# Kernel optimization log

Hardware: AMD Instinct MI355X
Metric: run time of the kernel (lower is better)

Reference implementation:

```python
import jax, jax.numpy as jnp
import numpy as np

B, D, K, H, W = 2, 512, 32, 64, 64


def setup_inputs() -> dict:
    key = jax.random.key(0)
    k1, k2, k3 = jax.random.split(key, 3)
    X = jax.random.normal(k1, (B, D, H, W), dtype=jnp.float32)
    std1 = 1.0 / (K * D) ** 0.5
    codewords = jax.random.uniform(k2, (K, D), minval=-std1, maxval=std1, dtype=jnp.float32)
    scale = jax.random.uniform(k3, (D, K), minval=-1.0, maxval=0.0, dtype=jnp.float32)
    return {"X": X, "codewords": codewords, "scale": scale}


def reference(X, codewords, scale):
    # X: [B, D, H, W] -> x: [B, N, D], N = H*W
    Bv, Dv = X.shape[0], X.shape[1]
    x = X.reshape(Bv, Dv, -1).transpose(0, 2, 1)            # [B, N, D]
    # broadcast residual: x[b,n,d] - codewords[k,d], scaled per (d,k)
    residual = (x[:, :, :, None] - codewords.T) * scale     # [B, N, D, K]
    # soft assignment over K codewords
    Q = jax.nn.softmax(-0.5 * jnp.sum(residual * residual, axis=2), axis=2)  # [B, N, K]
    # weighted aggregation over N, normalized by per-codeword mass
    Z_num = jnp.einsum('bnk,bndk->bdk', Q, residual)        # [B, D, K]
    Z_ = Z_num / Q.sum(axis=1)[:, None, :]                  # [B, D, K]
    # L2-normalize along D
    Z = Z_ / jnp.sqrt(jnp.sum(Z_ * Z_, axis=1, keepdims=True))
    return (Z, Q)
```

## Files before the change

kernel.cpp:

```cpp
#include <hip/hip_runtime.h>
#include <math.h>

#define B_DIM 2
#define D_DIM 512
#define K_DIM 32
#define N_DIM 4096

typedef float v2f __attribute__((ext_vector_type(2)));

__device__ __forceinline__ void pk_bl(v2f& d, v2f a, v2f b) {
    asm("v_pk_fma_f32 %0, %1, %2, %0 op_sel:[0,0,0] op_sel_hi:[1,0,1]"
        : "+v"(d) : "v"(a), "v"(b));
}
__device__ __forceinline__ void pk_bh(v2f& d, v2f a, v2f b) {
    asm("v_pk_fma_f32 %0, %1, %2, %0 op_sel:[0,1,0] op_sel_hi:[1,1,1]"
        : "+v"(d) : "v"(a), "v"(b));
}

__global__ __launch_bounds__(256)
void k_prep(const float* __restrict__ CW, const float* __restrict__ SC,
            float* __restrict__ A, float* __restrict__ B2,
            float* __restrict__ CK, float* __restrict__ zeroes)
{
    __shared__ float ckred[8][33];
    const int tid = threadIdx.x;
    const int idx = blockIdx.x * 256 + tid;
    const int d = idx >> 5, k = idx & 31;
    float s = SC[idx];
    float c = CW[k * D_DIM + d];
    float a = s * s;
    A[idx]  = a;
    B2[idx] = -2.f * a * c;
    if (blockIdx.x == 0) {
        if (tid < 128) zeroes[tid] = 0.f;
        const int kk = tid & 31, g = tid >> 5;
        float acc = 0.f;
        for (int dd = g * 64; dd < g * 64 + 64; ++dd) {
            float sv = SC[dd * K_DIM + kk];
            float cv = CW[kk * D_DIM + dd];
            acc = fmaf(sv * sv * cv, cv, acc);
        }
        ckred[g][kk] = acc;
        __syncthreads();
        if (tid < 32) {
            float t = 0.f;
#pragma unroll
            for (int i = 0; i < 8; ++i) t += ckred[i][tid];
            CK[tid] = t;
        }
    }
}

__global__ __launch_bounds__(256, 2)
void k_dist_q(const float* __restrict__ X, const float* __restrict__ At,
              const float* __restrict__ Bt, const float* __restrict__ CK,
              float* __restrict__ Qout)
{
    __shared__ __align__(16) float xlds[D_DIM * 16];
    __shared__ __align__(16) float part[8 * 16 * 36];

    const int tid = threadIdx.x;
    const int b  = blockIdx.x >> 8;
    const int n0 = (blockIdx.x & 255) << 4;

    const float* xsrc = X + (size_t)b * D_DIM * N_DIM + n0;
#pragma unroll
    for (int j = 0; j < 8; ++j) {
        const int d  = (tid >> 2) + (j << 6);
        const int n4 = (tid & 3) << 2;
        *(float4*)(&xlds[d * 16 + n4]) =
            *(const float4*)(xsrc + (size_t)d * N_DIM + n4);
    }

    const int ks  = tid & 7;
    const int ng  = (tid >> 3) & 3;
    const int dsl = tid >> 5;

    float acc[4][4];
#pragma unroll
    for (int n = 0; n < 4; ++n)
#pragma unroll
        for (int k = 0; k < 4; ++k) acc[n][k] = 0.f;

    const float* arow = At + ((dsl << 6) * K_DIM) + (ks << 2);
    const float* brow = Bt + ((dsl << 6) * K_DIM) + (ks << 2);
    __syncthreads();
    const float* xrow = &xlds[(dsl << 6) * 16 + (ng << 2)];

    for (int i = 0; i < 64; i += 8) {
#pragma unroll
        for (int u = 0; u < 8; ++u) {
            const int d = i + u;
            float4 a4 = *(const float4*)(arow + d * K_DIM);
            float4 b4 = *(const float4*)(brow + d * K_DIM);
            float4 x4 = *(const float4*)(xrow + d * 16);
            float av[4] = {a4.x, a4.y, a4.z, a4.w};
            float bv[4] = {b4.x, b4.y, b4.z, b4.w};
            float xv[4] = {x4.x, x4.y, x4.z, x4.w};
#pragma unroll
            for (int n = 0; n < 4; ++n) {
                const float x  = xv[n];
                const float x2 = x * x;
#pragma unroll
                for (int k = 0; k < 4; ++k)
                    acc[n][k] = fmaf(av[k], x2, fmaf(bv[k], x, acc[n][k]));
            }
        }
    }

    __syncthreads();
#pragma unroll
    for (int nj = 0; nj < 4; ++nj)
        *(float4*)(&part[(dsl * 16 + (ng << 2) + nj) * 36 + (ks << 2)]) =
            make_float4(acc[nj][0], acc[nj][1], acc[nj][2], acc[nj][3]);
    __syncthreads();

#pragma unroll
    for (int h = 0; h < 2; ++h) {
        const int n = (tid >> 5) + (h << 3);
        const int k = tid & 31;
        float dsum = CK[k];
#pragma unroll
        for (int i = 0; i < 8; ++i) dsum += part[(i * 16 + n) * 36 + k];
        float m = dsum;
#pragma unroll
        for (int mk = 16; mk >= 1; mk >>= 1)
            m = fminf(m, __shfl_xor(m, mk));
        float e = __expf(-0.5f * (dsum - m));
        float ssum = e;
#pragma unroll
        for (int mk = 16; mk >= 1; mk >>= 1)
            ssum += __shfl_xor(ssum, mk);
        Qout[((size_t)b * N_DIM + n0 + n) * K_DIM + k] = __fdividef(e, ssum);
    }
}

__global__ __launch_bounds__(256, 2)
void k_tpart(const float* __restrict__ X, const float* __restrict__ Qin,
             float* __restrict__ TP, float* __restrict__ Mpart)
{
    __shared__ __align__(16) float Xs[64 * 68];
    __shared__ __align__(16) float Qs[64 * 36];
    __shared__ __align__(16) float red4[4 * 64 * 36];
    __shared__ float mred[8][33];

    const int tid = threadIdx.x;
    const int bid = blockIdx.x;
    const int ns = bid & 31;
    const int dt = (bid >> 5) & 7;
    const int b  = bid >> 8;
    const int nsub = tid >> 5;
    const int dp = tid & 7;
    const int kp = (tid >> 3) & 3;
    const int k0t = kp << 3;
    const int wv = tid >> 6;

    v2f acc2[8][4];
#pragma unroll
    for (int i = 0; i < 8; ++i)
#pragma unroll
        for (int j = 0; j < 4; ++j) acc2[i][j] = (v2f)(0.f);

    const float* xsrc = X + ((size_t)b * D_DIM + dt * 64) * N_DIM + ns * 128;
    const float* qsrc = Qin + ((size_t)b * N_DIM + ns * 128) * K_DIM;

    for (int ch = 0; ch < 2; ++ch) {
        __syncthreads();
#pragma unroll
        for (int i = 0; i < 4; ++i) {
            int flat4 = tid + (i << 8);
            int row = flat4 >> 4;
            int c4  = (flat4 & 15) << 2;
            float4 v = *(const float4*)(xsrc + (size_t)row * N_DIM + (ch << 6) + c4);
            *(float4*)(&Xs[row * 68 + c4]) = v;
        }
#pragma unroll
        for (int i = 0; i < 2; ++i) {
            int flat4 = tid + (i << 8);
            int nn = flat4 >> 3;
            int k4 = (flat4 & 7) << 2;
            *(float4*)(&Qs[nn * 36 + k4]) =
                *(const float4*)(qsrc + ((ch << 6) + nn) * K_DIM + k4);
        }
        __syncthreads();
#pragma unroll
        for (int s = 0; s < 2; ++s) {
            const int nb = (nsub << 3) + (s << 2);
            float4 xr[8];
#pragma unroll
            for (int i = 0; i < 8; ++i)
                xr[i] = *(const float4*)(&Xs[(dp + (i << 3)) * 68 + nb]);
#pragma unroll
            for (int n = 0; n < 4; ++n) {
                float4 qa = *(const float4*)(&Qs[(nb + n) * 36 + k0t]);
                float4 qb = *(const float4*)(&Qs[(nb + n) * 36 + k0t + 4]);
                v2f q2[4] = {{qa.x, qa.y}, {qa.z, qa.w}, {qb.x, qb.y}, {qb.z, qb.w}};
#pragma unroll
                for (int i = 0; i < 8; ++i) {
                    v2f xlo = {xr[i].x, xr[i].y};
                    v2f xhi = {xr[i].z, xr[i].w};
                    v2f xb2 = (n < 2) ? xlo : xhi;
                    if ((n & 1) == 0) {
#pragma unroll
                        for (int j = 0; j < 4; ++j) pk_bl(acc2[i][j], q2[j], xb2);
                    } else {
#pragma unroll
                        for (int j = 0; j < 4; ++j) pk_bh(acc2[i][j], q2[j], xb2);
                    }
                }
            }
        }
    }
    __syncthreads();
#pragma unroll
    for (int i = 0; i < 8; ++i)
#pragma unroll
        for (int j = 0; j < 4; ++j) {
            acc2[i][j].x += __shfl_xor(acc2[i][j].x, 32);
            acc2[i][j].y += __shfl_xor(acc2[i][j].y, 32);
        }
    if ((tid & 32) == 0) {
#pragma unroll
        for (int i = 0; i < 8; ++i) {
            float* r = &red4[(wv * 64 + dp + (i << 3)) * 36 + k0t];
            *(float4*)(r)     = make_float4(acc2[i][0].x, acc2[i][0].y,
                                            acc2[i][1].x, acc2[i][1].y);
            *(float4*)(r + 4) = make_float4(acc2[i][2].x, acc2[i][2].y,
                                            acc2[i][3].x, acc2[i][3].y);
        }
    }
    __syncthreads();
    float* dst = TP + (((size_t)ns * 2 + b) * D_DIM + dt * 64) * K_DIM;
#pragma unroll
    for (int e = 0; e < 8; ++e) {
        int flat = tid + (e << 8);
        int dl = flat >> 5;
        int k  = flat & 31;
        float s = red4[(0 * 64 + dl) * 36 + k] + red4[(1 * 64 + dl) * 36 + k]
                + red4[(2 * 64 + dl) * 36 + k] + red4[(3 * 64 + dl) * 36 + k];
        dst[dl * K_DIM + k] = s;
    }
    if (dt == 0) {
        const int k = tid & 31, g = tid >> 5;
        float qm = 0.f;
#pragma unroll
        for (int n = 0; n < 16; ++n)
            qm += qsrc[(g * 16 + n) * K_DIM + k];
        mred[g][k] = qm;
        __syncthreads();
        if (tid < K_DIM) {
            float t = 0.f;
#pragma unroll
            for (int i = 0; i < 8; ++i) t += mred[i][tid];
            Mpart[(ns * B_DIM + b) * K_DIM + tid] = t;
        }
    }
}

__global__ __launch_bounds__(256)
void k_zfuse(const float* __restrict__ TP, const float* __restrict__ Mpart,
             const float* __restrict__ CW, const float* __restrict__ SC,
             float* __restrict__ Z, float* __restrict__ nsq, int* __restrict__ cnt)
{
    __shared__ float part[8][33];
    const int tid = threadIdx.x;
    const int b  = blockIdx.x >> 6;
    const int ds = blockIdx.x & 63;
    const int d  = (ds << 3) + (tid >> 5);
    const int k  = tid & 31;
    float sum = 0.f;
#pragma unroll
    for (int ns = 0; ns < 32; ++ns)
        sum += TP[(((size_t)ns * 2 + b) * D_DIM + d) * K_DIM + k];
    float m = 0.f;
#pragma unroll
    for (int ns = 0; ns < 32; ++ns)
        m += Mpart[(ns * B_DIM + b) * K_DIM + k];
    float c = CW[k * D_DIM + d];
    float s = SC[d * K_DIM + k];
    float z = s * (sum / m - c);
    part[tid >> 5][k] = z * z;
    __syncthreads();
    if (tid < K_DIM) {
        float t = 0.f;
#pragma unroll
        for (int i = 0; i < 8; ++i) t += part[i][tid];
        atomicAdd(&nsq[b * K_DIM + tid], t);
    }
    __syncthreads();
    if (tid == 0) {
        __hip_atomic_fetch_add(cnt, 1, __ATOMIC_ACQ_REL, __HIP_MEMORY_SCOPE_AGENT);
        while (__hip_atomic_load(cnt, __ATOMIC_ACQUIRE, __HIP_MEMORY_SCOPE_AGENT) < 128)
            __builtin_amdgcn_s_sleep(1);
    }
    __syncthreads();
    float nv = __hip_atomic_load(&nsq[b * K_DIM + k], __ATOMIC_RELAXED,
                                 __HIP_MEMORY_SCOPE_AGENT);
    Z[((b * D_DIM) + d) * K_DIM + k] = z * rsqrtf(nv);
}

extern "C" void kernel_launch(void* const* d_in, const int* in_sizes, int n_in,
                              void* d_out, int out_size, void* d_ws, size_t ws_size,
                              hipStream_t stream)
{
    const float* X  = (const float*)d_in[0];
    const float* CW = (const float*)d_in[1];
    const float* SC = (const float*)d_in[2];
    float* Z = (float*)d_out;
    float* Q = (float*)d_out + B_DIM * D_DIM * K_DIM;

    float* W    = (float*)d_ws;
    float* nsq  = W;
    int*   cnt  = (int*)(W + 64);
    float* Mpart= W + 128;
    float* TP   = W + 128 + 2048;
    float* At   = TP + 32 * B_DIM * D_DIM * K_DIM;
    float* Bt   = At + D_DIM * K_DIM;
    float* CKt  = Bt + D_DIM * K_DIM;

    k_prep  <<< 64, 256, 0, stream>>>(CW, SC, At, Bt, CKt, W);
    k_dist_q<<<512, 256, 0, stream>>>(X, At, Bt, CKt, Q);
    k_tpart <<<512, 256, 0, stream>>>(X, Q, TP, Mpart);
    k_zfuse <<<128, 256, 0, stream>>>(TP, Mpart, CW, SC, Z, nsq, cnt);
}
```

Before: 102.8 us.

## Split distance kernel into D-sliced partial pass plus separate softmax kernel

The fused distance-plus-softmax kernel is split in two. The first kernel computes partial squared distances over 64-row D slabs for 64-point N tiles, with smaller LDS use and higher occupancy, and writes 8 partial slabs to a workspace buffer. A new softmax kernel sums those slabs, applies the softmax, writes Q and computes the per-codeword mass partials that k_tpart used to compute. This trades extra global traffic (about 8 MB of partials written and read back) and one more launch for better occupancy and less redundant A/B reloads in the distance pass.

```diff
diff --git a/kernel.cpp b/kernel.cpp
--- a/kernel.cpp
+++ b/kernel.cpp
@@ -51,30 +51,36 @@
     }
 }
 
-__global__ __launch_bounds__(256, 2)
-void k_dist_q(const float* __restrict__ X, const float* __restrict__ At,
-              const float* __restrict__ Bt, const float* __restrict__ CK,
-              float* __restrict__ Qout)
-{
-    __shared__ __align__(16) float xlds[D_DIM * 16];
-    __shared__ __align__(16) float part[8 * 16 * 36];
-
-    const int tid = threadIdx.x;
+__global__ __launch_bounds__(256, 4)
+void k_dist(const float* __restrict__ X, const float* __restrict__ At,
+            const float* __restrict__ Bt, float* __restrict__ DB)
+{
+    __shared__ __align__(16) float xs[128 * 68];
+
+    const int tid = threadIdx.x;
+    const int nb = blockIdx.x & 63;
+    const int dc = (blockIdx.x >> 6) & 3;
     const int b  = blockIdx.x >> 8;
-    const int n0 = (blockIdx.x & 255) << 4;
-
-    const float* xsrc = X + (size_t)b * D_DIM * N_DIM + n0;
-#pragma unroll
-    for (int j = 0; j < 8; ++j) {
-        const int d  = (tid >> 2) + (j << 6);
-        const int n4 = (tid & 3) << 2;
-        *(float4*)(&xlds[d * 16 + n4]) =
-            *(const float4*)(xsrc + (size_t)d * N_DIM + n4);
-    }
-
-    const int ks  = tid & 7;
-    const int ng  = (tid >> 3) & 3;
-    const int dsl = tid >> 5;
+
+    const float* xsrc = X + ((size_t)b * D_DIM + dc * 128) * N_DIM + nb * 64;
+#pragma unroll
+    for (int i = 0; i < 8; ++i) {
+        int flat4 = tid + (i << 8);
+        int row  = flat4 >> 4;
+        int col4 = (flat4 & 15) << 2;
+        *(float4*)(&xs[row * 68 + col4]) =
+            *(const float4*)(xsrc + (size_t)row * N_DIM + col4);
+    }
+    __syncthreads();
+
+    const int ks = tid & 7;
+    const int ng = (tid >> 3) & 15;
+    const int dh = tid >> 7;
+    const int d0 = dc * 128 + dh * 64;
+
+    const float* ar = At + d0 * K_DIM + (ks << 2);
+    const float* br = Bt + d0 * K_DIM + (ks << 2);
+    const float* xr = &xs[(dh << 6) * 68 + (ng << 2)];
 
     float acc[4][4];
 #pragma unroll
@@ -82,67 +88,80 @@
 #pragma unroll
         for (int k = 0; k < 4; ++k) acc[n][k] = 0.f;
 
-    const float* arow = At + ((dsl << 6) * K_DIM) + (ks << 2);
-    const float* brow = Bt + ((dsl << 6) * K_DIM) + (ks << 2);
-    __syncthreads();
-    const float* xrow = &xlds[(dsl << 6) * 16 + (ng << 2)];
-
-    for (int i = 0; i < 64; i += 8) {
-#pragma unroll
-        for (int u = 0; u < 8; ++u) {
-            const int d = i + u;
-            float4 a4 = *(const float4*)(arow + d * K_DIM);
-            float4 b4 = *(const float4*)(brow + d * K_DIM);
-            float4 x4 = *(const float4*)(xrow + d * 16);
-            float av[4] = {a4.x, a4.y, a4.z, a4.w};
-            float bv[4] = {b4.x, b4.y, b4.z, b4.w};
-            float xv[4] = {x4.x, x4.y, x4.z, x4.w};
-#pragma unroll
-            for (int n = 0; n < 4; ++n) {
-                const float x  = xv[n];
-                const float x2 = x * x;
-#pragma unroll
-                for (int k = 0; k < 4; ++k)
-                    acc[n][k] = fmaf(av[k], x2, fmaf(bv[k], x, acc[n][k]));
-            }
-        }
-    }
-
-    __syncthreads();
-#pragma unroll
-    for (int nj = 0; nj < 4; ++nj)
-        *(float4*)(&part[(dsl * 16 + (ng << 2) + nj) * 36 + (ks << 2)]) =
-            make_float4(acc[nj][0], acc[nj][1], acc[nj][2], acc[nj][3]);
-    __syncthreads();
-
-#pragma unroll
-    for (int h = 0; h < 2; ++h) {
-        const int n = (tid >> 5) + (h << 3);
-        const int k = tid & 31;
-        float dsum = CK[k];
-#pragma unroll
-        for (int i = 0; i < 8; ++i) dsum += part[(i * 16 + n) * 36 + k];
-        float m = dsum;
+#pragma unroll 8
+    for (int d = 0; d < 64; ++d) {
+        float4 a4 = *(const float4*)(ar + d * K_DIM);
+        float4 b4 = *(const float4*)(br + d * K_DIM);
+        float4 x4 = *(const float4*)(xr + d * 68);
+        float av[4] = {a4.x, a4.y, a4.z, a4.w};
+        float bv[4] = {b4.x, b4.y, b4.z, b4.w};
+        float xv[4] = {x4.x, x4.y, x4.z, x4.w};
+#pragma unroll
+        for (int n = 0; n < 4; ++n) {
+            const float x  = xv[n];
+            const float x2 = x * x;
+#pragma unroll
+            for (int k = 0; k < 4; ++k)
+                acc[n][k] = fmaf(av[k], x2, fmaf(bv[k], x, acc[n][k]));
+        }
+    }
+
+    const int slab = dc * 2 + dh;
+    float* dst = DB + (((size_t)slab * B_DIM + b) * N_DIM + nb * 64 + (ng << 2))
+                    * K_DIM + (ks << 2);
+#pragma unroll
+    for (int nn = 0; nn < 4; ++nn)
+        *(float4*)(dst + nn * K_DIM) =
+            make_float4(acc[nn][0], acc[nn][1], acc[nn][2], acc[nn][3]);
+}
+
+__global__ __launch_bounds__(256)
+void k_softmax(const float* __restrict__ DB, const float* __restrict__ CK,
+               float* __restrict__ Qout, float* __restrict__ Mpart)
+{
+    __shared__ float mred[8][33];
+    const int tid = threadIdx.x;
+    const int b  = blockIdx.x >> 6;
+    const int nb = blockIdx.x & 63;
+    const int k = tid & 31, g = tid >> 5;
+    float qm = 0.f;
+#pragma unroll
+    for (int p = 0; p < 8; ++p) {
+        const int n = nb * 64 + p * 8 + g;
+        float s = CK[k];
+#pragma unroll
+        for (int sl = 0; sl < 8; ++sl)
+            s += DB[(((size_t)sl * B_DIM + b) * N_DIM + n) * K_DIM + k];
+        float m = s;
 #pragma unroll
         for (int mk = 16; mk >= 1; mk >>= 1)
             m = fminf(m, __shfl_xor(m, mk));
-        float e = __expf(-0.5f * (dsum - m));
+        float e = __expf(-0.5f * (s - m));
         float ssum = e;
 #pragma unroll
         for (int mk = 16; mk >= 1; mk >>= 1)
             ssum += __shfl_xor(ssum, mk);
-        Qout[((size_t)b * N_DIM + n0 + n) * K_DIM + k] = __fdividef(e, ssum);
+        float q = __fdividef(e, ssum);
+        Qout[((size_t)b * N_DIM + n) * K_DIM + k] = q;
+        qm += q;
+    }
+    mred[g][k] = qm;
+    __syncthreads();
+    if (tid < K_DIM) {
+        float t = 0.f;
+#pragma unroll
+        for (int i = 0; i < 8; ++i) t += mred[i][tid];
+        Mpart[blockIdx.x * K_DIM + tid] = t;
     }
 }
 
 __global__ __launch_bounds__(256, 2)
 void k_tpart(const float* __restrict__ X, const float* __restrict__ Qin,
-             float* __restrict__ TP, float* __restrict__ Mpart)
+             float* __restrict__ TP)
 {
     __shared__ __align__(16) float Xs[64 * 68];
     __shared__ __align__(16) float Qs[64 * 36];
     __shared__ __align__(16) float red4[4 * 64 * 36];
-    __shared__ float mred[8][33];
 
     const int tid = threadIdx.x;
     const int bid = blockIdx.x;
@@ -240,21 +259,6 @@
                 + red4[(2 * 64 + dl) * 36 + k] + red4[(3 * 64 + dl) * 36 + k];
         dst[dl * K_DIM + k] = s;
     }
-    if (dt == 0) {
-        const int k = tid & 31, g = tid >> 5;
-        float qm = 0.f;
-#pragma unroll
-        for (int n = 0; n < 16; ++n)
-            qm += qsrc[(g * 16 + n) * K_DIM + k];
-        mred[g][k] = qm;
-        __syncthreads();
-        if (tid < K_DIM) {
-            float t = 0.f;
-#pragma unroll
-            for (int i = 0; i < 8; ++i) t += mred[i][tid];
-            Mpart[(ns * B_DIM + b) * K_DIM + tid] = t;
-        }
-    }
 }
 
 __global__ __launch_bounds__(256)
@@ -274,8 +278,8 @@
         sum += TP[(((size_t)ns * 2 + b) * D_DIM + d) * K_DIM + k];
     float m = 0.f;
 #pragma unroll
-    for (int ns = 0; ns < 32; ++ns)
-        m += Mpart[(ns * B_DIM + b) * K_DIM + k];
+    for (int i = 0; i < 64; ++i)
+        m += Mpart[((b << 6) + i) * K_DIM + k];
     float c = CW[k * D_DIM + d];
     float s = SC[d * K_DIM + k];
     float z = s * (sum / m - c);
@@ -313,13 +317,15 @@
     float* nsq  = W;
     int*   cnt  = (int*)(W + 64);
     float* Mpart= W + 128;
-    float* TP   = W + 128 + 2048;
-    float* At   = TP + 32 * B_DIM * D_DIM * K_DIM;
+    float* TP   = Mpart + 4096;
+    float* DB   = TP + 32 * B_DIM * D_DIM * K_DIM;
+    float* At   = DB + 8 * B_DIM * N_DIM * K_DIM;
     float* Bt   = At + D_DIM * K_DIM;
     float* CKt  = Bt + D_DIM * K_DIM;
 
-    k_prep  <<< 64, 256, 0, stream>>>(CW, SC, At, Bt, CKt, W);
-    k_dist_q<<<512, 256, 0, stream>>>(X, At, Bt, CKt, Q);
-    k_tpart <<<512, 256, 0, stream>>>(X, Q, TP, Mpart);
-    k_zfuse <<<128, 256, 0, stream>>>(TP, Mpart, CW, SC, Z, nsq, cnt);
-}
+    k_prep   <<< 64, 256, 0, stream>>>(CW, SC, At, Bt, CKt, W);
+    k_dist   <<<512, 256, 0, stream>>>(X, At, Bt, DB);
+    k_softmax<<<128, 256, 0, stream>>>(DB, CKt, Q, Mpart);
+    k_tpart  <<<512, 256, 0, stream>>>(X, Q, TP);
+    k_zfuse  <<<128, 256, 0, stream>>>(TP, Mpart, CW, SC, Z, nsq, cnt);
+}
```

Measured after the change: 106.4 us. 1.04x slower.

## Fuse distance/softmax, aggregation and normalization into one persistent kernel with grid barriers

Applied to the files above, without the earlier changes.

Merges the three main kernels (distance plus softmax, Q-weighted aggregation, and Z normalization) into a single 256-block persistent kernel separated by atomic-counter grid barriers. The per-codeword mass is now accumulated atomically during the softmax stage instead of being reduced separately. Each block handles 32 tokens in the first phase and two aggregation tiles in the second. This removes two kernel launches and their gaps, at the cost of lower occupancy (one block per CU), spin-wait barriers that assume all 256 blocks are co-resident, and a non-deterministic order for the atomic reductions.

```diff
diff --git a/kernel.cpp b/kernel.cpp
--- a/kernel.cpp
+++ b/kernel.cpp
@@ -17,10 +17,20 @@
         : "+v"(d) : "v"(a), "v"(b));
 }
 
+__device__ __forceinline__ void gridbar(int* cnt, int target) {
+    __syncthreads();
+    if (threadIdx.x == 0) {
+        __hip_atomic_fetch_add(cnt, 1, __ATOMIC_ACQ_REL, __HIP_MEMORY_SCOPE_AGENT);
+        while (__hip_atomic_load(cnt, __ATOMIC_ACQUIRE, __HIP_MEMORY_SCOPE_AGENT) < target)
+            __builtin_amdgcn_s_sleep(2);
+    }
+    __syncthreads();
+}
+
 __global__ __launch_bounds__(256)
 void k_prep(const float* __restrict__ CW, const float* __restrict__ SC,
             float* __restrict__ A, float* __restrict__ B2,
-            float* __restrict__ CK, float* __restrict__ zeroes)
+            float* __restrict__ CK, float* __restrict__ W)
 {
     __shared__ float ckred[8][33];
     const int tid = threadIdx.x;
@@ -32,7 +42,7 @@
     A[idx]  = a;
     B2[idx] = -2.f * a * c;
     if (blockIdx.x == 0) {
-        if (tid < 128) zeroes[tid] = 0.f;
+        if (tid < 136) W[tid] = 0.f;
         const int kk = tid & 31, g = tid >> 5;
         float acc = 0.f;
         for (int dd = g * 64; dd < g * 64 + 64; ++dd) {
@@ -51,49 +61,48 @@
     }
 }
 
-__global__ __launch_bounds__(256, 2)
-void k_dist_q(const float* __restrict__ X, const float* __restrict__ At,
-              const float* __restrict__ Bt, const float* __restrict__ CK,
-              float* __restrict__ Qout)
+__global__ __launch_bounds__(256, 1)
+void k_mega(const float* __restrict__ X, const float* __restrict__ CW,
+            const float* __restrict__ SC, const float* __restrict__ At,
+            const float* __restrict__ Bt, const float* __restrict__ CK,
+            float* __restrict__ Qout, float* __restrict__ Z,
+            float* __restrict__ W, float* __restrict__ TP)
 {
-    __shared__ __align__(16) float xlds[D_DIM * 16];
-    __shared__ __align__(16) float part[8 * 16 * 36];
-
+    __shared__ __align__(16) float sm[18432];
+    float* Mv  = W;
+    float* nsq = W + 64;
+    int*   cnt = (int*)(W + 128);
     const int tid = threadIdx.x;
-    const int b  = blockIdx.x >> 8;
-    const int n0 = (blockIdx.x & 255) << 4;
-
-    const float* xsrc = X + (size_t)b * D_DIM * N_DIM + n0;
-#pragma unroll
-    for (int j = 0; j < 8; ++j) {
-        const int d  = (tid >> 2) + (j << 6);
-        const int n4 = (tid & 3) << 2;
-        *(float4*)(&xlds[d * 16 + n4]) =
-            *(const float4*)(xsrc + (size_t)d * N_DIM + n4);
-    }
-
-    const int ks  = tid & 7;
-    const int ng  = (tid >> 3) & 3;
-    const int dsl = tid >> 5;
-
-    float acc[4][4];
-#pragma unroll
-    for (int n = 0; n < 4; ++n)
-#pragma unroll
-        for (int k = 0; k < 4; ++k) acc[n][k] = 0.f;
-
-    const float* arow = At + ((dsl << 6) * K_DIM) + (ks << 2);
-    const float* brow = Bt + ((dsl << 6) * K_DIM) + (ks << 2);
-    __syncthreads();
-    const float* xrow = &xlds[(dsl << 6) * 16 + (ng << 2)];
-
-    for (int i = 0; i < 64; i += 8) {
-#pragma unroll
-        for (int u = 0; u < 8; ++u) {
-            const int d = i + u;
-            float4 a4 = *(const float4*)(arow + d * K_DIM);
-            float4 b4 = *(const float4*)(brow + d * K_DIM);
-            float4 x4 = *(const float4*)(xrow + d * 16);
+    const int blk = blockIdx.x;
+
+    {
+        const int b  = blk >> 7;
+        const int n0 = (blk & 127) << 5;
+        const float* xsrc = X + (size_t)b * D_DIM * N_DIM + n0;
+#pragma unroll
+        for (int i = 0; i < 16; ++i) {
+            int f4 = tid + (i << 8);
+            int row = f4 >> 3, col4 = (f4 & 7) << 2;
+            *(float4*)(&sm[row * 36 + col4]) =
+                *(const float4*)(xsrc + (size_t)row * N_DIM + col4);
+        }
+        __syncthreads();
+
+        const int ks = tid & 7, ng = (tid >> 3) & 7, dh = tid >> 6;
+        const float* ar = At + (dh << 7) * K_DIM + (ks << 2);
+        const float* br = Bt + (dh << 7) * K_DIM + (ks << 2);
+        const float* xr = &sm[(dh << 7) * 36 + (ng << 2)];
+        float acc[4][4];
+#pragma unroll
+        for (int n = 0; n < 4; ++n)
+#pragma unroll
+            for (int k = 0; k < 4; ++k) acc[n][k] = 0.f;
+
+#pragma unroll 8
+        for (int d = 0; d < 128; ++d) {
+            float4 a4 = *(const float4*)(ar + d * K_DIM);
+            float4 b4 = *(const float4*)(br + d * K_DIM);
+            float4 x4 = *(const float4*)(xr + d * 36);
             float av[4] = {a4.x, a4.y, a4.z, a4.w};
             float bv[4] = {b4.x, b4.y, b4.z, b4.w};
             float xv[4] = {x4.x, x4.y, x4.z, x4.w};
@@ -106,197 +115,187 @@
                     acc[n][k] = fmaf(av[k], x2, fmaf(bv[k], x, acc[n][k]));
             }
         }
-    }
-
-    __syncthreads();
-#pragma unroll
-    for (int nj = 0; nj < 4; ++nj)
-        *(float4*)(&part[(dsl * 16 + (ng << 2) + nj) * 36 + (ks << 2)]) =
-            make_float4(acc[nj][0], acc[nj][1], acc[nj][2], acc[nj][3]);
-    __syncthreads();
-
-#pragma unroll
-    for (int h = 0; h < 2; ++h) {
-        const int n = (tid >> 5) + (h << 3);
+        __syncthreads();
+#pragma unroll
+        for (int nj = 0; nj < 4; ++nj)
+            *(float4*)(&sm[((dh << 5) + (ng << 2) + nj) * 36 + (ks << 2)]) =
+                make_float4(acc[nj][0], acc[nj][1], acc[nj][2], acc[nj][3]);
+        __syncthreads();
+
         const int k = tid & 31;
-        float dsum = CK[k];
-#pragma unroll
-        for (int i = 0; i < 8; ++i) dsum += part[(i * 16 + n) * 36 + k];
-        float m = dsum;
-#pragma unroll
-        for (int mk = 16; mk >= 1; mk >>= 1)
-            m = fminf(m, __shfl_xor(m, mk));
-        float e = __expf(-0.5f * (dsum - m));
-        float ssum = e;
-#pragma unroll
-        for (int mk = 16; mk >= 1; mk >>= 1)
-            ssum += __shfl_xor(ssum, mk);
-        Qout[((size_t)b * N_DIM + n0 + n) * K_DIM + k] = __fdividef(e, ssum);
-    }
-}
-
-__global__ __launch_bounds__(256, 2)
-void k_tpart(const float* __restrict__ X, const float* __restrict__ Qin,
-             float* __restrict__ TP, float* __restrict__ Mpart)
-{
-    __shared__ __align__(16) float Xs[64 * 68];
-    __shared__ __align__(16) float Qs[64 * 36];
-    __shared__ __align__(16) float red4[4 * 64 * 36];
-    __shared__ float mred[8][33];
-
-    const int tid = threadIdx.x;
-    const int bid = blockIdx.x;
-    const int ns = bid & 31;
-    const int dt = (bid >> 5) & 7;
-    const int b  = bid >> 8;
-    const int nsub = tid >> 5;
-    const int dp = tid & 7;
-    const int kp = (tid >> 3) & 3;
-    const int k0t = kp << 3;
-    const int wv = tid >> 6;
-
-    v2f acc2[8][4];
-#pragma unroll
-    for (int i = 0; i < 8; ++i)
-#pragma unroll
-        for (int j = 0; j < 4; ++j) acc2[i][j] = (v2f)(0.f);
-
-    const float* xsrc = X + ((size_t)b * D_DIM + dt * 64) * N_DIM + ns * 128;
-    const float* qsrc = Qin + ((size_t)b * N_DIM + ns * 128) * K_DIM;
-
-    for (int ch = 0; ch < 2; ++ch) {
-        __syncthreads();
-#pragma unroll
-        for (int i = 0; i < 4; ++i) {
-            int flat4 = tid + (i << 8);
-            int row = flat4 >> 4;
-            int c4  = (flat4 & 15) << 2;
-            float4 v = *(const float4*)(xsrc + (size_t)row * N_DIM + (ch << 6) + c4);
-            *(float4*)(&Xs[row * 68 + c4]) = v;
-        }
-#pragma unroll
-        for (int i = 0; i < 2; ++i) {
-            int flat4 = tid + (i << 8);
-            int nn = flat4 >> 3;
-            int k4 = (flat4 & 7) << 2;
-            *(float4*)(&Qs[nn * 36 + k4]) =
-                *(const float4*)(qsrc + ((ch << 6) + nn) * K_DIM + k4);
-        }
-        __syncthreads();
-#pragma unroll
-        for (int s = 0; s < 2; ++s) {
-            const int nb = (nsub << 3) + (s << 2);
-            float4 xr[8];
-#pragma unroll
-            for (int i = 0; i < 8; ++i)
-                xr[i] = *(const float4*)(&Xs[(dp + (i << 3)) * 68 + nb]);
-#pragma unroll
-            for (int n = 0; n < 4; ++n) {
-                float4 qa = *(const float4*)(&Qs[(nb + n) * 36 + k0t]);
-                float4 qb = *(const float4*)(&Qs[(nb + n) * 36 + k0t + 4]);
-                v2f q2[4] = {{qa.x, qa.y}, {qa.z, qa.w}, {qb.x, qb.y}, {qb.z, qb.w}};
-#pragma unroll
-                for (int i = 0; i < 8; ++i) {
-                    v2f xlo = {xr[i].x, xr[i].y};
-                    v2f xhi = {xr[i].z, xr[i].w};
-                    v2f xb2 = (n < 2) ? xlo : xhi;
-                    if ((n & 1) == 0) {
-#pragma unroll
-                        for (int j = 0; j < 4; ++j) pk_bl(acc2[i][j], q2[j], xb2);
-                    } else {
-#pragma unroll
-                        for (int j = 0; j < 4; ++j) pk_bh(acc2[i][j], q2[j], xb2);
-                    }
-                }
-            }
-        }
-    }
-    __syncthreads();
-#pragma unroll
-    for (int i = 0; i < 8; ++i)
-#pragma unroll
-        for (int j = 0; j < 4; ++j) {
-            acc2[i][j].x += __shfl_xor(acc2[i][j].x, 32);
-            acc2[i][j].y += __shfl_xor(acc2[i][j].y, 32);
-        }
-    if ((tid & 32) == 0) {
-#pragma unroll
-        for (int i = 0; i < 8; ++i) {
-            float* r = &red4[(wv * 64 + dp + (i << 3)) * 36 + k0t];
-            *(float4*)(r)     = make_float4(acc2[i][0].x, acc2[i][0].y,
-                                            acc2[i][1].x, acc2[i][1].y);
-            *(float4*)(r + 4) = make_float4(acc2[i][2].x, acc2[i][2].y,
-                                            acc2[i][3].x, acc2[i][3].y);
-        }
-    }
-    __syncthreads();
-    float* dst = TP + (((size_t)ns * 2 + b) * D_DIM + dt * 64) * K_DIM;
-#pragma unroll
-    for (int e = 0; e < 8; ++e) {
-        int flat = tid + (e << 8);
-        int dl = flat >> 5;
-        int k  = flat & 31;
-        float s = red4[(0 * 64 + dl) * 36 + k] + red4[(1 * 64 + dl) * 36 + k]
-                + red4[(2 * 64 + dl) * 36 + k] + red4[(3 * 64 + dl) * 36 + k];
-        dst[dl * K_DIM + k] = s;
-    }
-    if (dt == 0) {
-        const int k = tid & 31, g = tid >> 5;
         float qm = 0.f;
 #pragma unroll
-        for (int n = 0; n < 16; ++n)
-            qm += qsrc[(g * 16 + n) * K_DIM + k];
-        mred[g][k] = qm;
+        for (int h = 0; h < 4; ++h) {
+            const int n = (h << 3) + (tid >> 5);
+            float dsum = CK[k];
+#pragma unroll
+            for (int i = 0; i < 4; ++i) dsum += sm[((i << 5) + n) * 36 + k];
+            float m = dsum;
+#pragma unroll
+            for (int mk = 16; mk >= 1; mk >>= 1)
+                m = fminf(m, __shfl_xor(m, mk));
+            float e = __expf(-0.5f * (dsum - m));
+            float ssum = e;
+#pragma unroll
+            for (int mk = 16; mk >= 1; mk >>= 1)
+                ssum += __shfl_xor(ssum, mk);
+            float q = __fdividef(e, ssum);
+            Qout[((size_t)b * N_DIM + n0 + n) * K_DIM + k] = q;
+            qm += q;
+        }
+        sm[4608 + (tid >> 5) * 33 + k] = qm;
         __syncthreads();
         if (tid < K_DIM) {
             float t = 0.f;
 #pragma unroll
-            for (int i = 0; i < 8; ++i) t += mred[i][tid];
-            Mpart[(ns * B_DIM + b) * K_DIM + tid] = t;
-        }
-    }
-}
-
-__global__ __launch_bounds__(256)
-void k_zfuse(const float* __restrict__ TP, const float* __restrict__ Mpart,
-             const float* __restrict__ CW, const float* __restrict__ SC,
-             float* __restrict__ Z, float* __restrict__ nsq, int* __restrict__ cnt)
-{
-    __shared__ float part[8][33];
-    const int tid = threadIdx.x;
-    const int b  = blockIdx.x >> 6;
-    const int ds = blockIdx.x & 63;
-    const int d  = (ds << 3) + (tid >> 5);
-    const int k  = tid & 31;
-    float sum = 0.f;
-#pragma unroll
-    for (int ns = 0; ns < 32; ++ns)
-        sum += TP[(((size_t)ns * 2 + b) * D_DIM + d) * K_DIM + k];
-    float m = 0.f;
-#pragma unroll
-    for (int ns = 0; ns < 32; ++ns)
-        m += Mpart[(ns * B_DIM + b) * K_DIM + k];
-    float c = CW[k * D_DIM + d];
-    float s = SC[d * K_DIM + k];
-    float z = s * (sum / m - c);
-    part[tid >> 5][k] = z * z;
-    __syncthreads();
-    if (tid < K_DIM) {
+            for (int i = 0; i < 8; ++i) t += sm[4608 + i * 33 + tid];
+            atomicAdd(&Mv[b * K_DIM + tid], t);
+        }
+    }
+    gridbar(&cnt[0], 256);
+
+    {
+        float* Xs   = sm;
+        float* Qs   = sm + 4352;
+        float* red4 = sm + 6656;
+        const int nsub = tid >> 5;
+        const int dp = tid & 7;
+        const int kp = (tid >> 3) & 3;
+        const int k0t = kp << 3;
+        const int wv = tid >> 6;
+
+        for (int a = 0; a < 2; ++a) {
+            const int g  = (blk << 1) | a;
+            const int ns = g & 31;
+            const int dt = (g >> 5) & 7;
+            const int b  = g >> 8;
+
+            v2f acc2[8][4];
+#pragma unroll
+            for (int i = 0; i < 8; ++i)
+#pragma unroll
+                for (int j = 0; j < 4; ++j) acc2[i][j] = (v2f)(0.f);
+
+            const float* xsrc = X + ((size_t)b * D_DIM + dt * 64) * N_DIM + ns * 128;
+            const float* qsrc = Qout + ((size_t)b * N_DIM + ns * 128) * K_DIM;
+
+            for (int ch = 0; ch < 2; ++ch) {
+                __syncthreads();
+#pragma unroll
+                for (int i = 0; i < 4; ++i) {
+                    int flat4 = tid + (i << 8);
+                    int row = flat4 >> 4;
+                    int c4  = (flat4 & 15) << 2;
+                    *(float4*)(&Xs[row * 68 + c4]) =
+                        *(const float4*)(xsrc + (size_t)row * N_DIM + (ch << 6) + c4);
+                }
+#pragma unroll
+                for (int i = 0; i < 2; ++i) {
+                    int flat4 = tid + (i << 8);
+                    int nn = flat4 >> 3;
+                    int k4 = (flat4 & 7) << 2;
+                    *(float4*)(&Qs[nn * 36 + k4]) =
+                        *(const float4*)(qsrc + ((ch << 6) + nn) * K_DIM + k4);
+                }
+                __syncthreads();
+#pragma unroll
+                for (int s = 0; s < 2; ++s) {
+                    const int nb = (nsub << 3) + (s << 2);
+                    float4 xr[8];
+#pragma unroll
+                    for (int i = 0; i < 8; ++i)
+                        xr[i] = *(const float4*)(&Xs[(dp + (i << 3)) * 68 + nb]);
+#pragma unroll
+                    for (int n = 0; n < 4; ++n) {
+                        float4 qa = *(const float4*)(&Qs[(nb + n) * 36 + k0t]);
+                        float4 qb = *(const float4*)(&Qs[(nb + n) * 36 + k0t + 4]);
+                        v2f q2[4] = {{qa.x, qa.y}, {qa.z, qa.w},
+                                     {qb.x, qb.y}, {qb.z, qb.w}};
+#pragma unroll
+                        for (int i = 0; i < 8; ++i) {
+                            v2f xlo = {xr[i].x, xr[i].y};
+                            v2f xhi = {xr[i].z, xr[i].w};
+                            v2f xb2 = (n < 2) ? xlo : xhi;
+                            if ((n & 1) == 0) {
+#pragma unroll
+                                for (int j = 0; j < 4; ++j) pk_bl(acc2[i][j], q2[j], xb2);
+                            } else {
+#pragma unroll
+                                for (int j = 0; j < 4; ++j) pk_bh(acc2[i][j], q2[j], xb2);
+                            }
+                        }
+                    }
+                }
+            }
+            __syncthreads();
+#pragma unroll
+            for (int i = 0; i < 8; ++i)
+#pragma unroll
+                for (int j = 0; j < 4; ++j) {
+                    acc2[i][j].x += __shfl_xor(acc2[i][j].x, 32);
+                    acc2[i][j].y += __shfl_xor(acc2[i][j].y, 32);
+                }
+            if ((tid & 32) == 0) {
+#pragma unroll
+                for (int i = 0; i < 8; ++i) {
+                    float* r = &red4[(wv * 64 + dp + (i << 3)) * 36 + k0t];
+                    *(float4*)(r)     = make_float4(acc2[i][0].x, acc2[i][0].y,
+                                                    acc2[i][1].x, acc2[i][1].y);
+                    *(float4*)(r + 4) = make_float4(acc2[i][2].x, acc2[i][2].y,
+                                                    acc2[i][3].x, acc2[i][3].y);
+                }
+            }
+            __syncthreads();
+            float* dst = TP + (((size_t)ns * 2 + b) * D_DIM + dt * 64) * K_DIM;
+#pragma unroll
+            for (int e = 0; e < 8; ++e) {
+                int flat = tid + (e << 8);
+                int dl = flat >> 5;
+                int k  = flat & 31;
+                float s = red4[(0 * 64 + dl) * 36 + k] + red4[(1 * 64 + dl) * 36 + k]
+                        + red4[(2 * 64 + dl) * 36 + k] + red4[(3 * 64 + dl) * 36 + k];
+                dst[dl * K_DIM + k] = s;
+            }
+        }
+    }
+    gridbar(&cnt[1], 256);
+
+    {
+        const int b   = blk >> 7;
+        const int d0  = (blk & 127) << 2;
+        const int k   = tid & 31;
+        const int dd  = (tid >> 5) & 3;
+        const int h   = tid >> 7;
         float t = 0.f;
 #pragma unroll
-        for (int i = 0; i < 8; ++i) t += part[i][tid];
-        atomicAdd(&nsq[b * K_DIM + tid], t);
-    }
-    __syncthreads();
-    if (tid == 0) {
-        __hip_atomic_fetch_add(cnt, 1, __ATOMIC_ACQ_REL, __HIP_MEMORY_SCOPE_AGENT);
-        while (__hip_atomic_load(cnt, __ATOMIC_ACQUIRE, __HIP_MEMORY_SCOPE_AGENT) < 128)
-            __builtin_amdgcn_s_sleep(1);
-    }
-    __syncthreads();
-    float nv = __hip_atomic_load(&nsq[b * K_DIM + k], __ATOMIC_RELAXED,
-                                 __HIP_MEMORY_SCOPE_AGENT);
-    Z[((b * D_DIM) + d) * K_DIM + k] = z * rsqrtf(nv);
+        for (int s = 0; s < 16; ++s) {
+            int slab = (h << 4) + s;
+            t += TP[(((size_t)slab * B_DIM + b) * D_DIM + d0 + dd) * K_DIM + k];
+        }
+        sm[((dd << 1) + h) * 33 + k] = t;
+        __syncthreads();
+        float z = 0.f;
+        if (h == 0) {
+            float T = sm[(dd << 1) * 33 + k] + sm[((dd << 1) + 1) * 33 + k];
+            float m = Mv[b * K_DIM + k];
+            float c = CW[k * D_DIM + d0 + dd];
+            float s2 = SC[(d0 + dd) * K_DIM + k];
+            z = s2 * (__fdividef(T, m) - c);
+            sm[300 + dd * 33 + k] = z * z;
+        }
+        __syncthreads();
+        if (tid < K_DIM) {
+            float nn = sm[300 + tid] + sm[300 + 33 + tid]
+                     + sm[300 + 66 + tid] + sm[300 + 99 + tid];
+            atomicAdd(&nsq[b * K_DIM + tid], nn);
+        }
+        gridbar(&cnt[2], 256);
+        if (h == 0) {
+            float nv = __hip_atomic_load(&nsq[b * K_DIM + k], __ATOMIC_RELAXED,
+                                         __HIP_MEMORY_SCOPE_AGENT);
+            Z[((size_t)b * D_DIM + d0 + dd) * K_DIM + k] = z * rsqrtf(nv);
+        }
+    }
 }
 
 extern "C" void kernel_launch(void* const* d_in, const int* in_sizes, int n_in,
@@ -309,17 +308,12 @@
     float* Z = (float*)d_out;
     float* Q = (float*)d_out + B_DIM * D_DIM * K_DIM;
 
-    float* W    = (float*)d_ws;
-    float* nsq  = W;
-    int*   cnt  = (int*)(W + 64);
-    float* Mpart= W + 128;
-    float* TP   = W + 128 + 2048;
-    float* At   = TP + 32 * B_DIM * D_DIM * K_DIM;
-    float* Bt   = At + D_DIM * K_DIM;
-    float* CKt  = Bt + D_DIM * K_DIM;
-
-    k_prep  <<< 64, 256, 0, stream>>>(CW, SC, At, Bt, CKt, W);
-    k_dist_q<<<512, 256, 0, stream>>>(X, At, Bt, CKt, Q);
-    k_tpart <<<512, 256, 0, stream>>>(X, Q, TP, Mpart);
-    k_zfuse <<<128, 256, 0, stream>>>(TP, Mpart, CW, SC, Z, nsq, cnt);
-}
+    float* W   = (float*)d_ws;
+    float* TP  = W + 256;
+    float* At  = TP + 32 * B_DIM * D_DIM * K_DIM;
+    float* Bt  = At + D_DIM * K_DIM;
+    float* CKt = Bt + D_DIM * K_DIM;
+
+    k_prep<<< 64, 256, 0, stream>>>(CW, SC, At, Bt, CKt, W);
+    k_mega<<<256, 256, 0, stream>>>(X, CW, SC, At, Bt, CKt, Q, Z, W, TP);
+}
```

Measured after the change: 144.3 us. +40.3%, slower.

## Stage A/B tables in LDS per D-chunk, widen k-tile, fuse Q mass into distq

Applied to the files above, without the earlier changes.

The distance kernel now streams X, A and B in four 128-row D chunks through shared memory, and each thread computes a 4x8 (n,k) tile across 16 D-slices. Previously only X was staged, the whole slab at once, and A/B came from global memory with 4x4 tiles. The per-codeword Q mass is now reduced inside the distance kernel instead of re-reading Q in k_tpart, which gives 256 per-block partials that k_zfuse sums. This trades more syncs and a longer final reduction for less global traffic, smaller LDS footprint and higher arithmetic intensity per thread.

```diff
diff --git a/kernel.cpp b/kernel.cpp
--- a/kernel.cpp
+++ b/kernel.cpp
@@ -20,7 +20,7 @@
 __global__ __launch_bounds__(256)
 void k_prep(const float* __restrict__ CW, const float* __restrict__ SC,
             float* __restrict__ A, float* __restrict__ B2,
-            float* __restrict__ CK, float* __restrict__ zeroes)
+            float* __restrict__ CK, float* __restrict__ W)
 {
     __shared__ float ckred[8][33];
     const int tid = threadIdx.x;
@@ -32,7 +32,7 @@
     A[idx]  = a;
     B2[idx] = -2.f * a * c;
     if (blockIdx.x == 0) {
-        if (tid < 128) zeroes[tid] = 0.f;
+        if (tid < 136) W[tid] = 0.f;
         const int kk = tid & 31, g = tid >> 5;
         float acc = 0.f;
         for (int dd = g * 64; dd < g * 64 + 64; ++dd) {
@@ -52,57 +52,71 @@
 }
 
 __global__ __launch_bounds__(256, 2)
-void k_dist_q(const float* __restrict__ X, const float* __restrict__ At,
-              const float* __restrict__ Bt, const float* __restrict__ CK,
-              float* __restrict__ Qout)
-{
-    __shared__ __align__(16) float xlds[D_DIM * 16];
-    __shared__ __align__(16) float part[8 * 16 * 36];
+void k_distq(const float* __restrict__ X, const float* __restrict__ At,
+             const float* __restrict__ Bt, const float* __restrict__ CK,
+             float* __restrict__ Qout, float* __restrict__ Mpart)
+{
+    __shared__ __align__(16) float sm[10624];
+    float* Al = sm;
+    float* Bl = sm + 4224;
+    float* Xl = sm + 8448;
+    float* part = sm;
 
     const int tid = threadIdx.x;
     const int b  = blockIdx.x >> 8;
     const int n0 = (blockIdx.x & 255) << 4;
 
+    const int ks = tid & 3;
+    const int ng = (tid >> 2) & 3;
+    const int dh = tid >> 4;
+
+    float acc[4][8];
+#pragma unroll
+    for (int n = 0; n < 4; ++n)
+#pragma unroll
+        for (int k = 0; k < 8; ++k) acc[n][k] = 0.f;
+
     const float* xsrc = X + (size_t)b * D_DIM * N_DIM + n0;
-#pragma unroll
-    for (int j = 0; j < 8; ++j) {
-        const int d  = (tid >> 2) + (j << 6);
-        const int n4 = (tid & 3) << 2;
-        *(float4*)(&xlds[d * 16 + n4]) =
-            *(const float4*)(xsrc + (size_t)d * N_DIM + n4);
-    }
-
-    const int ks  = tid & 7;
-    const int ng  = (tid >> 3) & 3;
-    const int dsl = tid >> 5;
-
-    float acc[4][4];
-#pragma unroll
-    for (int n = 0; n < 4; ++n)
-#pragma unroll
-        for (int k = 0; k < 4; ++k) acc[n][k] = 0.f;
-
-    const float* arow = At + ((dsl << 6) * K_DIM) + (ks << 2);
-    const float* brow = Bt + ((dsl << 6) * K_DIM) + (ks << 2);
-    __syncthreads();
-    const float* xrow = &xlds[(dsl << 6) * 16 + (ng << 2)];
-
-    for (int i = 0; i < 64; i += 8) {
+
+    for (int c = 0; c < 4; ++c) {
+        __syncthreads();
+#pragma unroll
+        for (int i = 0; i < 4; ++i) {
+            int f4 = tid + (i << 8);
+            int row = f4 >> 3, c4 = (f4 & 7) << 2;
+            *(float4*)(&Al[row * 33 + c4]) =
+                *(const float4*)(At + ((c << 7) + row) * K_DIM + c4);
+            *(float4*)(&Bl[row * 33 + c4]) =
+                *(const float4*)(Bt + ((c << 7) + row) * K_DIM + c4);
+        }
+#pragma unroll
+        for (int i = 0; i < 2; ++i) {
+            int f4 = tid + (i << 8);
+            int row = f4 >> 2, c4 = (f4 & 3) << 2;
+            *(float4*)(&Xl[row * 17 + c4]) =
+                *(const float4*)(xsrc + (size_t)((c << 7) + row) * N_DIM + c4);
+        }
+        __syncthreads();
+
+        const float* aL = &Al[(dh << 3) * 33 + (ks << 3)];
+        const float* bL = &Bl[(dh << 3) * 33 + (ks << 3)];
+        const float* xL = &Xl[(dh << 3) * 17 + (ng << 2)];
 #pragma unroll
         for (int u = 0; u < 8; ++u) {
-            const int d = i + u;
-            float4 a4 = *(const float4*)(arow + d * K_DIM);
-            float4 b4 = *(const float4*)(brow + d * K_DIM);
-            float4 x4 = *(const float4*)(xrow + d * 16);
-            float av[4] = {a4.x, a4.y, a4.z, a4.w};
-            float bv[4] = {b4.x, b4.y, b4.z, b4.w};
+            float4 a0 = *(const float4*)(aL + u * 33);
+            float4 a1 = *(const float4*)(aL + u * 33 + 4);
+            float4 b0 = *(const float4*)(bL + u * 33);
+            float4 b1 = *(const float4*)(bL + u * 33 + 4);
+            float4 x4 = *(const float4*)(xL + u * 17);
+            float av[8] = {a0.x, a0.y, a0.z, a0.w, a1.x, a1.y, a1.z, a1.w};
+            float bv[8] = {b0.x, b0.y, b0.z, b0.w, b1.x, b1.y, b1.z, b1.w};
             float xv[4] = {x4.x, x4.y, x4.z, x4.w};
 #pragma unroll
             for (int n = 0; n < 4; ++n) {
                 const float x  = xv[n];
                 const float x2 = x * x;
 #pragma unroll
-                for (int k = 0; k < 4; ++k)
+                for (int k = 0; k < 8; ++k)
                     acc[n][k] = fmaf(av[k], x2, fmaf(bv[k], x, acc[n][k]));
             }
         }
@@ -110,18 +124,21 @@
 
     __syncthreads();
 #pragma unroll
-    for (int nj = 0; nj < 4; ++nj)
-        *(float4*)(&part[(dsl * 16 + (ng << 2) + nj) * 36 + (ks << 2)]) =
-            make_float4(acc[nj][0], acc[nj][1], acc[nj][2], acc[nj][3]);
-    __syncthreads();
-
+    for (int nn = 0; nn < 4; ++nn) {
+        float* r = &part[((dh << 4) + (ng << 2) + nn) * 33 + (ks << 3)];
+        *(float4*)(r)     = make_float4(acc[nn][0], acc[nn][1], acc[nn][2], acc[nn][3]);
+        *(float4*)(r + 4) = make_float4(acc[nn][4], acc[nn][5], acc[nn][6], acc[nn][7]);
+    }
+    __syncthreads();
+
+    const int k = tid & 31;
+    float qm = 0.f;
 #pragma unroll
     for (int h = 0; h < 2; ++h) {
         const int n = (tid >> 5) + (h << 3);
-        const int k = tid & 31;
         float dsum = CK[k];
 #pragma unroll
-        for (int i = 0; i < 8; ++i) dsum += part[(i * 16 + n) * 36 + k];
+        for (int i = 0; i < 16; ++i) dsum += part[((i << 4) + n) * 33 + k];
         float m = dsum;
 #pragma unroll
         for (int mk = 16; mk >= 1; mk >>= 1)
@@ -131,18 +148,28 @@
 #pragma unroll
         for (int mk = 16; mk >= 1; mk >>= 1)
             ssum += __shfl_xor(ssum, mk);
-        Qout[((size_t)b * N_DIM + n0 + n) * K_DIM + k] = __fdividef(e, ssum);
+        float q = __fdividef(e, ssum);
+        Qout[((size_t)b * N_DIM + n0 + n) * K_DIM + k] = q;
+        qm += q;
+    }
+    float* mred = Xl;
+    mred[(tid >> 5) * 33 + k] = qm;
+    __syncthreads();
+    if (tid < K_DIM) {
+        float t = 0.f;
+#pragma unroll
+        for (int i = 0; i < 8; ++i) t += mred[i * 33 + tid];
+        Mpart[blockIdx.x * K_DIM + tid] = t;
     }
 }
 
 __global__ __launch_bounds__(256, 2)
 void k_tpart(const float* __restrict__ X, const float* __restrict__ Qin,
-             float* __restrict__ TP, float* __restrict__ Mpart)
+             float* __restrict__ TP)
 {
     __shared__ __align__(16) float Xs[64 * 68];
     __shared__ __align__(16) float Qs[64 * 36];
     __shared__ __align__(16) float red4[4 * 64 * 36];
-    __shared__ float mred[8][33];
 
     const int tid = threadIdx.x;
     const int bid = blockIdx.x;
@@ -171,8 +198,8 @@
             int flat4 = tid + (i << 8);
             int row = flat4 >> 4;
             int c4  = (flat4 & 15) << 2;
-            float4 v = *(const float4*)(xsrc + (size_t)row * N_DIM + (ch << 6) + c4);
-            *(float4*)(&Xs[row * 68 + c4]) = v;
+            *(float4*)(&Xs[row * 68 + c4]) =
+                *(const float4*)(xsrc + (size_t)row * N_DIM + (ch << 6) + c4);
         }
 #pragma unroll
         for (int i = 0; i < 2; ++i) {
@@ -240,21 +267,6 @@
                 + red4[(2 * 64 + dl) * 36 + k] + red4[(3 * 64 + dl) * 36 + k];
         dst[dl * K_DIM + k] = s;
     }
-    if (dt == 0) {
-        const int k = tid & 31, g = tid >> 5;
-        float qm = 0.f;
-#pragma unroll
-        for (int n = 0; n < 16; ++n)
-            qm += qsrc[(g * 16 + n) * K_DIM + k];
-        mred[g][k] = qm;
-        __syncthreads();
-        if (tid < K_DIM) {
-            float t = 0.f;
-#pragma unroll
-            for (int i = 0; i < 8; ++i) t += mred[i][tid];
-            Mpart[(ns * B_DIM + b) * K_DIM + tid] = t;
-        }
-    }
 }
 
 __global__ __launch_bounds__(256)
@@ -273,12 +285,12 @@
     for (int ns = 0; ns < 32; ++ns)
         sum += TP[(((size_t)ns * 2 + b) * D_DIM + d) * K_DIM + k];
     float m = 0.f;
-#pragma unroll
-    for (int ns = 0; ns < 32; ++ns)
-        m += Mpart[(ns * B_DIM + b) * K_DIM + k];
+#pragma unroll 8
+    for (int i = 0; i < 256; ++i)
+        m += Mpart[((b << 8) + i) * K_DIM + k];
     float c = CW[k * D_DIM + d];
     float s = SC[d * K_DIM + k];
-    float z = s * (sum / m - c);
+    float z = s * (__fdividef(sum, m) - c);
     part[tid >> 5][k] = z * z;
     __syncthreads();
     if (tid < K_DIM) {
@@ -313,13 +325,13 @@
     float* nsq  = W;
     int*   cnt  = (int*)(W + 64);
     float* Mpart= W + 128;
-    float* TP   = W + 128 + 2048;
+    float* TP   = Mpart + 512 * K_DIM;
     float* At   = TP + 32 * B_DIM * D_DIM * K_DIM;
     float* Bt   = At + D_DIM * K_DIM;
     float* CKt  = Bt + D_DIM * K_DIM;
 
-    k_prep  <<< 64, 256, 0, stream>>>(CW, SC, At, Bt, CKt, W);
-    k_dist_q<<<512, 256, 0, stream>>>(X, At, Bt, CKt, Q);
-    k_tpart <<<512, 256, 0, stream>>>(X, Q, TP, Mpart);
-    k_zfuse <<<128, 256, 0, stream>>>(TP, Mpart, CW, SC, Z, nsq, cnt);
-}
+    k_prep <<< 64, 256, 0, stream>>>(CW, SC, At, Bt, CKt, W);
+    k_distq<<<512, 256, 0, stream>>>(X, At, Bt, CKt, Q, Mpart);
+    k_tpart<<<512, 256, 0, stream>>>(X, Q, TP);
+    k_zfuse<<<128, 256, 0, stream>>>(TP, Mpart, CW, SC, Z, nsq, cnt);
+}
```

Result: slower. 133.6 us (+29.9%).
